# Performance work log

Hardware: AMD Instinct MI355X
Metric: run time of the kernel (lower is better)

The kernel has to match this reference:

```python
import jax, jax.numpy as jnp
import numpy as np

B = 2048          # batch
D = 256           # agent input dim
S = 32            # num_splines
CANVAS = 128      # canvas_size
NUM_T = 50        # samples along each Bezier curve (hard-coded in module)
BRUSH = 1         # brush_size (hard-coded)
SCALE = 1e-4      # Normal scale hard-coded in forward (log_std is unused)
W_STAMP = -0.07   # per-stamp weight (hard-coded)
BG = 0.3          # background_shade


def setup_inputs() -> dict:
    key = jax.random.key(0)
    k1, k2 = jax.random.split(key, 2)
    x = jax.random.normal(k1, (B, D), dtype=jnp.float32)
    W_agent = jax.random.normal(k2, (D, S * 6), dtype=jnp.float32) * 0.05
    b_agent = jnp.zeros((S * 6,), dtype=jnp.float32)
    return {"x": x, "W_agent": W_agent, "b_agent": b_agent}


def _paint_multiple_splines(sample):
    # sample: [B, S*6] in (0,1)
    bsz = sample.shape[0]
    params = sample.reshape(bsz, -1, 6) * CANVAS          # [B, S, 6]
    P0 = params[..., 0:2][:, :, None, :]                   # [B, S, 1, 2]
    P1 = params[..., 2:4][:, :, None, :]
    P2 = params[..., 4:6][:, :, None, :]
    t = jnp.linspace(0.0, 1.0, NUM_T, dtype=params.dtype).reshape(1, 1, NUM_T, 1)
    # quadratic Bezier: [B, S, T, 2]
    spline_points = (1 - t) ** 2 * P0 + 2 * (1 - t) * t * P1 + t ** 2 * P2
    coords = jnp.round(spline_points).astype(jnp.int32)
    r = jnp.arange(-BRUSH, BRUSH + 1)
    dx, dy = jnp.meshgrid(r, r, indexing="ij")
    dx, dy = dx.ravel(), dy.ravel()                        # [9]
    x_idx = jnp.clip(coords[..., 0][..., None] + dx, 0, CANVAS - 1)  # [B,S,T,9]
    y_idx = jnp.clip(coords[..., 1][..., None] + dy, 0, CANVAS - 1)
    flat_idx = (x_idx * CANVAS + y_idx).reshape(bsz, -1)   # [B, S*T*9]
    weights = jnp.full(flat_idx.shape, W_STAMP, dtype=jnp.float32)
    canvas_flat = jnp.zeros((bsz, CANVAS * CANVAS), dtype=jnp.float32)
    canvas_flat = canvas_flat.at[jnp.arange(bsz)[:, None], flat_idx].add(weights)
    canvas = canvas_flat.reshape(bsz, CANVAS, CANVAS)
    return jnp.clip(canvas + BG, 0.0, 1.0)


def reference(x, W_agent, b_agent):
    mu = x @ W_agent + b_agent                             # [B, S*6]
    scale = jnp.float32(SCALE)
    log2pi = jnp.log(jnp.float32(2.0) * jnp.pi)
    dim = mu.shape[-1]
    # eval-time path: raw_sample = mu
    raw = mu
    log_prob = jnp.sum(
        -0.5 * ((raw - mu) / scale) ** 2 - jnp.log(scale) - 0.5 * log2pi,
        axis=-1,
    )                                                      # [B]
    entropy = jnp.full(
        (mu.shape[0],), dim * (0.5 + 0.5 * log2pi + jnp.log(scale)),
        dtype=jnp.float32,
    )                                                      # [B]
    sample = jax.nn.sigmoid(raw)                           # [B, S*6]
    sketch = _paint_multiple_splines(sample)               # [B, CANVAS, CANVAS]
    return sketch, log_prob, entropy, sample
```

## Files before the change

kernel.cpp:

```cpp
#include <hip/hip_runtime.h>
#include <math.h>

#define NB      2048
#define DIM     256
#define SC6     192
#define CV      128
#define NT      50

#define LPV  (1591.9491530441301f)
#define ENV  (-1495.9491530441301f)

#define SKETCH_N   ((size_t)NB * CV * CV)
#define LP_OFF     (SKETCH_N)
#define ENT_OFF    (LP_OFF + NB)
#define SAMPLE_OFF (ENT_OFF + NB)

typedef float vfloat4 __attribute__((ext_vector_type(4)));

__global__ __launch_bounds__(512) void fused_kernel(
    const float* __restrict__ x, const float* __restrict__ W,
    const float* __restrict__ bias, float* __restrict__ out)
{
    __shared__ unsigned int cnt[CV * CV / 2];
    __shared__ double sp[6][32];
    __shared__ double cfa[NT], cfb[NT], cfc[NT];

    const int b   = blockIdx.x;
    const int tid = threadIdx.x;

    if (tid < SC6) {
        const int j = tid;
        const float* xb = x + (size_t)b * DIM;
        double acc = 0.0;
        #pragma unroll 8
        for (int d = 0; d < DIM; ++d) {
            acc = fma((double)xb[d], (double)W[d * SC6 + j], acc);
        }
        double mu = acc + (double)bias[j];
        double s  = 1.0 / (1.0 + exp(-mu));
        out[SAMPLE_OFF + (size_t)b * SC6 + j] = (float)s;
        sp[j % 6][j / 6] = s * 128.0;
    } else {
        const int t2 = tid - SC6;
        uint4* c4 = (uint4*)cnt;
        uint4 z = make_uint4(0u, 0u, 0u, 0u);
        for (int w = t2; w < 2048; w += 320) c4[w] = z;
        if (t2 < NT) {
            double t = (t2 == NT - 1) ? 1.0 : (double)t2 * (1.0 / 49.0);
            double u = 1.0 - t;
            cfa[t2] = u * u;
            cfb[t2] = (2.0 * u) * t;
            cfc[t2] = t * t;
        }
        if (t2 == 62) out[LP_OFF  + b] = LPV;
        if (t2 == 63) out[ENT_OFF + b] = ENV;
    }
    __syncthreads();

    for (int i = tid; i < 32 * NT; i += 512) {
        int s = i & 31;
        int k = i >> 5;
        double a  = cfa[k];
        double bq = cfb[k];
        double c  = cfc[k];
        double px = a * sp[0][s] + bq * sp[2][s] + c * sp[4][s];
        double py = a * sp[1][s] + bq * sp[3][s] + c * sp[5][s];
        int cx = (int)rint(px);
        int cy = (int)rint(py);

        int y0 = min(max(cy - 1, 0), CV - 1);
        int y1 = min(max(cy,     0), CV - 1);
        int y2 = min(max(cy + 1, 0), CV - 1);
        int cb = y0 >> 1;
        unsigned incA = 1u << ((y0 & 1) << 4);
        unsigned incB = 0u;
        unsigned i1 = 1u << ((y1 & 1) << 4);
        unsigned i2 = 1u << ((y2 & 1) << 4);
        if ((y1 >> 1) == cb) incA += i1; else incB += i1;
        if ((y2 >> 1) == cb) incA += i2; else incB += i2;

        int x0 = min(max(cx - 1, 0), CV - 1);
        int x1 = min(max(cx,     0), CV - 1);
        int x2 = min(max(cx + 1, 0), CV - 1);
        int rows[3] = {x0, x1, x2};
        #pragma unroll
        for (int r = 0; r < 3; ++r) {
            int xi = rows[r];
            int base = xi << 6;
            int sw = 3 * xi;
            atomicAdd(&cnt[base + ((cb + sw) & 63)], incA);
            if (incB) atomicAdd(&cnt[base + ((cb + 1 + sw) & 63)], incB);
        }
    }
    __syncthreads();

    vfloat4* ob = (vfloat4*)(out + (size_t)b * CV * CV);
    for (int w = tid; w < CV * CV / 4; w += 512) {
        int pb = w << 2;
        int xi = pb >> 7;
        int c0 = (pb >> 1) & 63;
        int base = xi << 6;
        int sw = 3 * xi;
        unsigned v0 = cnt[base + ((c0 + sw) & 63)];
        unsigned v1 = cnt[base + ((c0 + 1 + sw) & 63)];
        vfloat4 r;
        float f0 = 0.3f - 0.07f * (float)(v0 & 0xFFFFu);
        float f1 = 0.3f - 0.07f * (float)(v0 >> 16);
        float f2 = 0.3f - 0.07f * (float)(v1 & 0xFFFFu);
        float f3 = 0.3f - 0.07f * (float)(v1 >> 16);
        r.x = fminf(fmaxf(f0, 0.0f), 1.0f);
        r.y = fminf(fmaxf(f1, 0.0f), 1.0f);
        r.z = fminf(fmaxf(f2, 0.0f), 1.0f);
        r.w = fminf(fmaxf(f3, 0.0f), 1.0f);
        __builtin_nontemporal_store(r, &ob[w]);
    }
}

extern "C" void kernel_launch(void* const* d_in, const int* in_sizes, int n_in,
                              void* d_out, int out_size, void* d_ws, size_t ws_size,
                              hipStream_t stream) {
    const float* x    = (const float*)d_in[0];
    const float* W    = (const float*)d_in[1];
    const float* bias = (const float*)d_in[2];
    float* out = (float*)d_out;

    fused_kernel<<<NB, 512, 0, stream>>>(x, W, bias, out);
}
```

Before: 171.2 us.

## Process two batch rows per block with 8-bit packed LDS counters

Each block now handles two batch rows, so every W load feeds two fp64 FMA chains, and it paints the two canvases one after the other, reusing the LDS counter buffer. The LDS counters are packed four 8-bit values per word instead of two 16-bit ones, which halves shared memory and the initial clear. The buffer is re-zeroed while it is read out for the next canvas. This halves the grid and adds more serial work per block. The 8-bit counters could overflow if more than 255 stamps hit one pixel, which is possible with 1600 points and 9 stamps each if many curves overlap.

```diff
diff --git a/kernel.cpp b/kernel.cpp
--- a/kernel.cpp
+++ b/kernel.cpp
@@ -6,6 +6,7 @@
 #define SC6     192
 #define CV      128
 #define NT      50
+#define NBPB    2
 
 #define LPV  (1591.9491530441301f)
 #define ENV  (-1495.9491530441301f)
@@ -21,30 +22,36 @@
     const float* __restrict__ x, const float* __restrict__ W,
     const float* __restrict__ bias, float* __restrict__ out)
 {
-    __shared__ unsigned int cnt[CV * CV / 2];
-    __shared__ double sp[6][32];
+    __shared__ unsigned int cnt[CV * CV / 4];
+    __shared__ double sp[NBPB][6][32];
     __shared__ double cfa[NT], cfb[NT], cfc[NT];
 
-    const int b   = blockIdx.x;
+    const int b0  = blockIdx.x * NBPB;
     const int tid = threadIdx.x;
 
     if (tid < SC6) {
         const int j = tid;
-        const float* xb = x + (size_t)b * DIM;
-        double acc = 0.0;
+        const float* xb0 = x + (size_t)b0 * DIM;
+        const float* xb1 = xb0 + DIM;
+        double a0 = 0.0, a1 = 0.0;
         #pragma unroll 8
         for (int d = 0; d < DIM; ++d) {
-            acc = fma((double)xb[d], (double)W[d * SC6 + j], acc);
+            double wd = (double)W[d * SC6 + j];
+            a0 = fma((double)xb0[d], wd, a0);
+            a1 = fma((double)xb1[d], wd, a1);
         }
-        double mu = acc + (double)bias[j];
-        double s  = 1.0 / (1.0 + exp(-mu));
-        out[SAMPLE_OFF + (size_t)b * SC6 + j] = (float)s;
-        sp[j % 6][j / 6] = s * 128.0;
+        double bj = (double)bias[j];
+        double s0 = 1.0 / (1.0 + exp(-(a0 + bj)));
+        double s1 = 1.0 / (1.0 + exp(-(a1 + bj)));
+        out[SAMPLE_OFF + (size_t)b0 * SC6 + j]       = (float)s0;
+        out[SAMPLE_OFF + (size_t)(b0 + 1) * SC6 + j] = (float)s1;
+        sp[0][j % 6][j / 6] = s0 * 128.0;
+        sp[1][j % 6][j / 6] = s1 * 128.0;
     } else {
         const int t2 = tid - SC6;
         uint4* c4 = (uint4*)cnt;
         uint4 z = make_uint4(0u, 0u, 0u, 0u);
-        for (int w = t2; w < 2048; w += 320) c4[w] = z;
+        for (int w = t2; w < 1024; w += 320) c4[w] = z;
         if (t2 < NT) {
             double t = (t2 == NT - 1) ? 1.0 : (double)t2 * (1.0 / 49.0);
             double u = 1.0 - t;
@@ -52,67 +59,65 @@
             cfb[t2] = (2.0 * u) * t;
             cfc[t2] = t * t;
         }
-        if (t2 == 62) out[LP_OFF  + b] = LPV;
-        if (t2 == 63) out[ENT_OFF + b] = ENV;
+        if (t2 == 60) out[LP_OFF  + b0]     = LPV;
+        if (t2 == 61) out[ENT_OFF + b0]     = ENV;
+        if (t2 == 62) out[LP_OFF  + b0 + 1] = LPV;
+        if (t2 == 63) out[ENT_OFF + b0 + 1] = ENV;
     }
     __syncthreads();
 
-    for (int i = tid; i < 32 * NT; i += 512) {
-        int s = i & 31;
-        int k = i >> 5;
-        double a  = cfa[k];
-        double bq = cfb[k];
-        double c  = cfc[k];
-        double px = a * sp[0][s] + bq * sp[2][s] + c * sp[4][s];
-        double py = a * sp[1][s] + bq * sp[3][s] + c * sp[5][s];
-        int cx = (int)rint(px);
-        int cy = (int)rint(py);
+    #pragma unroll
+    for (int bb = 0; bb < NBPB; ++bb) {
+        for (int i = tid; i < 32 * NT; i += 512) {
+            int s = i & 31;
+            int k = i >> 5;
+            double a  = cfa[k];
+            double bq = cfb[k];
+            double c  = cfc[k];
+            double px = a * sp[bb][0][s] + bq * sp[bb][2][s] + c * sp[bb][4][s];
+            double py = a * sp[bb][1][s] + bq * sp[bb][3][s] + c * sp[bb][5][s];
+            int cx = (int)rint(px);
+            int cy = (int)rint(py);
 
-        int y0 = min(max(cy - 1, 0), CV - 1);
-        int y1 = min(max(cy,     0), CV - 1);
-        int y2 = min(max(cy + 1, 0), CV - 1);
-        int cb = y0 >> 1;
-        unsigned incA = 1u << ((y0 & 1) << 4);
-        unsigned incB = 0u;
-        unsigned i1 = 1u << ((y1 & 1) << 4);
-        unsigned i2 = 1u << ((y2 & 1) << 4);
-        if ((y1 >> 1) == cb) incA += i1; else incB += i1;
-        if ((y2 >> 1) == cb) incA += i2; else incB += i2;
+            int y0 = min(max(cy - 1, 0), CV - 1);
+            int y1 = min(max(cy,     0), CV - 1);
+            int y2 = min(max(cy + 1, 0), CV - 1);
+            int cb = y0 >> 2;
+            unsigned incA = 1u << ((y0 & 3) << 3);
+            unsigned incB = 0u;
+            unsigned i1 = 1u << ((y1 & 3) << 3);
+            unsigned i2 = 1u << ((y2 & 3) << 3);
+            if ((y1 >> 2) == cb) incA += i1; else incB += i1;
+            if ((y2 >> 2) == cb) incA += i2; else incB += i2;
 
-        int x0 = min(max(cx - 1, 0), CV - 1);
-        int x1 = min(max(cx,     0), CV - 1);
-        int x2 = min(max(cx + 1, 0), CV - 1);
-        int rows[3] = {x0, x1, x2};
-        #pragma unroll
-        for (int r = 0; r < 3; ++r) {
-            int xi = rows[r];
-            int base = xi << 6;
-            int sw = 3 * xi;
-            atomicAdd(&cnt[base + ((cb + sw) & 63)], incA);
-            if (incB) atomicAdd(&cnt[base + ((cb + 1 + sw) & 63)], incB);
+            int x0 = min(max(cx - 1, 0), CV - 1);
+            int x1 = min(max(cx,     0), CV - 1);
+            int x2 = min(max(cx + 1, 0), CV - 1);
+            int rows[3] = {x0, x1, x2};
+            #pragma unroll
+            for (int r = 0; r < 3; ++r) {
+                int xi = rows[r];
+                int base = xi << 5;
+                atomicAdd(&cnt[base + ((cb + xi) & 31)], incA);
+                if (incB) atomicAdd(&cnt[base + ((cb + 1 + xi) & 31)], incB);
+            }
         }
-    }
-    __syncthreads();
+        __syncthreads();
 
-    vfloat4* ob = (vfloat4*)(out + (size_t)b * CV * CV);
-    for (int w = tid; w < CV * CV / 4; w += 512) {
-        int pb = w << 2;
-        int xi = pb >> 7;
-        int c0 = (pb >> 1) & 63;
-        int base = xi << 6;
-        int sw = 3 * xi;
-        unsigned v0 = cnt[base + ((c0 + sw) & 63)];
-        unsigned v1 = cnt[base + ((c0 + 1 + sw) & 63)];
-        vfloat4 r;
-        float f0 = 0.3f - 0.07f * (float)(v0 & 0xFFFFu);
-        float f1 = 0.3f - 0.07f * (float)(v0 >> 16);
-        float f2 = 0.3f - 0.07f * (float)(v1 & 0xFFFFu);
-        float f3 = 0.3f - 0.07f * (float)(v1 >> 16);
-        r.x = fminf(fmaxf(f0, 0.0f), 1.0f);
-        r.y = fminf(fmaxf(f1, 0.0f), 1.0f);
-        r.z = fminf(fmaxf(f2, 0.0f), 1.0f);
-        r.w = fminf(fmaxf(f3, 0.0f), 1.0f);
-        __builtin_nontemporal_store(r, &ob[w]);
+        vfloat4* ob = (vfloat4*)(out + (size_t)(b0 + bb) * CV * CV);
+        for (int w = tid; w < CV * CV / 4; w += 512) {
+            int xi  = w >> 5;
+            int idx = (xi << 5) + (((w & 31) + xi) & 31);
+            unsigned v = cnt[idx];
+            cnt[idx] = 0u;
+            vfloat4 r;
+            r.x = fminf(fmaxf(0.3f - 0.07f * (float)( v        & 255u), 0.0f), 1.0f);
+            r.y = fminf(fmaxf(0.3f - 0.07f * (float)((v >>  8) & 255u), 0.0f), 1.0f);
+            r.z = fminf(fmaxf(0.3f - 0.07f * (float)((v >> 16) & 255u), 0.0f), 1.0f);
+            r.w = fminf(fmaxf(0.3f - 0.07f * (float)( v >> 24        ), 0.0f), 1.0f);
+            __builtin_nontemporal_store(r, &ob[w]);
+        }
+        if (bb + 1 < NBPB) __syncthreads();
     }
 }
 
@@ -124,5 +129,5 @@
     const float* bias = (const float*)d_in[2];
     float* out = (float*)d_out;
 
-    fused_kernel<<<NB, 512, 0, stream>>>(x, W, bias, out);
+    fused_kernel<<<NB / NBPB, 512, 0, stream>>>(x, W, bias, out);
 }
```

Result: faster. 163.8 us (-4.3%).
